# Kernel tuning notes

Hardware: AMD Instinct MI355X
Metric: run time of the kernel (lower is better)

## Reference

```python
import jax, jax.numpy as jnp
import numpy as np

NUM_WORDS = 100000
D_IN = 256

def setup_inputs() -> dict:
    key = jax.random.key(0)
    k1, k2 = jax.random.split(key)
    x = jax.random.normal(k1, (NUM_WORDS, D_IN), dtype=jnp.float32)
    # neighbor indices in [-1, NUM_WORDS); -1 means 'no neighbor' (masked out)
    indices = jax.random.randint(k2, (NUM_WORDS, 4), -1, NUM_WORDS, dtype=jnp.int64)
    return {"x": x, "indices": indices}

def reference(x, indices):
    # x: [N, D], indices: [N, 4] int (-1 -> masked neighbor)
    mask = (indices != -1)                               # [N, 4]
    safe_idx = jnp.maximum(indices, 0)                   # clamp -1 -> 0 like np.maximum in source
    gathered = x[safe_idx]                               # [N, 4, D]
    gathered = gathered * mask[..., None].astype(x.dtype)
    n, d = x.shape
    return jnp.concatenate([x, gathered.reshape(n, 4 * d)], axis=1)  # [N, 5*D]
```

## Files before the change

### kernel.cpp

```cpp
#include <hip/hip_runtime.h>


typedef float f32x4 __attribute__((ext_vector_type(4)));

#define D 256
#define D4 (D / 4)
#define OUTW (5 * D)
#define OUTW4 (OUTW / 4)
#define ROWS_PER_BLOCK 4

__global__ __launch_bounds__(256) void collect_kernel(
    const f32x4* __restrict__ x4,
    const int*   __restrict__ indices,
    f32x4*       __restrict__ out4,
    int n)
{
    const int wave = threadIdx.x >> 6;
    const int lane = threadIdx.x & 63;
    const int row  = blockIdx.x * ROWS_PER_BLOCK + wave;
    if (row >= n) return;

    const f32x4* xrow = x4 + (long)row * D4;
    f32x4* orow = out4 + (long)row * OUTW4;

    const int i0 = indices[row * 4 + 0];
    const int i1 = indices[row * 4 + 1];
    const int i2 = indices[row * 4 + 2];
    const int i3 = indices[row * 4 + 3];

    const f32x4 zero = (f32x4){0.f, 0.f, 0.f, 0.f};

    f32x4 v_self = __builtin_nontemporal_load(&xrow[lane]);
    f32x4 v0 = (i0 >= 0) ? x4[(long)i0 * D4 + lane] : zero;
    f32x4 v1 = (i1 >= 0) ? x4[(long)i1 * D4 + lane] : zero;
    f32x4 v2 = (i2 >= 0) ? x4[(long)i2 * D4 + lane] : zero;
    f32x4 v3 = (i3 >= 0) ? x4[(long)i3 * D4 + lane] : zero;

    __builtin_nontemporal_store(v_self, &orow[lane]);
    __builtin_nontemporal_store(v0, &orow[D4 * 1 + lane]);
    __builtin_nontemporal_store(v1, &orow[D4 * 2 + lane]);
    __builtin_nontemporal_store(v2, &orow[D4 * 3 + lane]);
    __builtin_nontemporal_store(v3, &orow[D4 * 4 + lane]);
}

extern "C" void kernel_launch(void* const* d_in, const int* in_sizes, int n_in,
                              void* d_out, int out_size, void* d_ws, size_t ws_size,
                              hipStream_t stream)
{
    const f32x4* x4 = (const f32x4*)d_in[0];
    const int* indices = (const int*)d_in[1];
    f32x4* out4 = (f32x4*)d_out;

    const int n = in_sizes[0] / D;

    dim3 block(256);
    dim3 grid((n + ROWS_PER_BLOCK - 1) / ROWS_PER_BLOCK);
    collect_kernel<<<grid, block, 0, stream>>>(x4, indices, out4, n);
}
```

Before: 150.8 us.

## Split gather into two passes over source-row halves for cache locality

Splits the gather into two kernel launches. Each launch only gathers neighbor rows whose index falls in one half of x, so the working set of gathered rows (about 51 MB per half) has a better chance of staying in the last-level cache. The first pass also copies the self rows and writes zeros for masked neighbors. The cost is a second launch, reading the indices twice, and more divergent branches per wave.

```diff
diff --git a/kernel.cpp b/kernel.cpp
--- a/kernel.cpp
+++ b/kernel.cpp
@@ -5,42 +5,56 @@
 
 #define D 256
 #define D4 (D / 4)
-#define OUTW (5 * D)
-#define OUTW4 (OUTW / 4)
+#define OUTW4 (5 * D / 4)
 #define ROWS_PER_BLOCK 4
 
-__global__ __launch_bounds__(256) void collect_kernel(
+__global__ __launch_bounds__(256) void collect_pass_kernel(
     const f32x4* __restrict__ x4,
     const int*   __restrict__ indices,
     f32x4*       __restrict__ out4,
-    int n)
+    int n, int seg_lo, int seg_hi, int do_self)
 {
     const int wave = threadIdx.x >> 6;
     const int lane = threadIdx.x & 63;
     const int row  = blockIdx.x * ROWS_PER_BLOCK + wave;
     if (row >= n) return;
 
-    const f32x4* xrow = x4 + (long)row * D4;
     f32x4* orow = out4 + (long)row * OUTW4;
 
-    const int i0 = indices[row * 4 + 0];
-    const int i1 = indices[row * 4 + 1];
-    const int i2 = indices[row * 4 + 2];
-    const int i3 = indices[row * 4 + 3];
+    int idx[4];
+    idx[0] = indices[row * 4 + 0];
+    idx[1] = indices[row * 4 + 1];
+    idx[2] = indices[row * 4 + 2];
+    idx[3] = indices[row * 4 + 3];
 
     const f32x4 zero = (f32x4){0.f, 0.f, 0.f, 0.f};
 
-    f32x4 v_self = __builtin_nontemporal_load(&xrow[lane]);
-    f32x4 v0 = (i0 >= 0) ? x4[(long)i0 * D4 + lane] : zero;
-    f32x4 v1 = (i1 >= 0) ? x4[(long)i1 * D4 + lane] : zero;
-    f32x4 v2 = (i2 >= 0) ? x4[(long)i2 * D4 + lane] : zero;
-    f32x4 v3 = (i3 >= 0) ? x4[(long)i3 * D4 + lane] : zero;
+    if (do_self) {
+        const f32x4* xrow = x4 + (long)row * D4;
+        f32x4 v_self;
+        if (row >= seg_lo && row < seg_hi) {
+            v_self = xrow[lane];
+        } else {
+            v_self = __builtin_nontemporal_load(&xrow[lane]);
+        }
+        __builtin_nontemporal_store(v_self, &orow[lane]);
 
-    __builtin_nontemporal_store(v_self, &orow[lane]);
-    __builtin_nontemporal_store(v0, &orow[D4 * 1 + lane]);
-    __builtin_nontemporal_store(v1, &orow[D4 * 2 + lane]);
-    __builtin_nontemporal_store(v2, &orow[D4 * 3 + lane]);
-    __builtin_nontemporal_store(v3, &orow[D4 * 4 + lane]);
+        #pragma unroll
+        for (int s = 0; s < 4; ++s) {
+            if (idx[s] < 0) {
+                __builtin_nontemporal_store(zero, &orow[D4 * (1 + s) + lane]);
+            }
+        }
+    }
+
+    #pragma unroll
+    for (int s = 0; s < 4; ++s) {
+        const int t = idx[s];
+        if (t >= seg_lo && t < seg_hi) {
+            f32x4 v = x4[(long)t * D4 + lane];
+            __builtin_nontemporal_store(v, &orow[D4 * (1 + s) + lane]);
+        }
+    }
 }
 
 extern "C" void kernel_launch(void* const* d_in, const int* in_sizes, int n_in,
@@ -52,8 +66,13 @@
     f32x4* out4 = (f32x4*)d_out;
 
     const int n = in_sizes[0] / D;
+    const int half = n / 2;
 
     dim3 block(256);
     dim3 grid((n + ROWS_PER_BLOCK - 1) / ROWS_PER_BLOCK);
-    collect_kernel<<<grid, block, 0, stream>>>(x4, indices, out4, n);
+
+    collect_pass_kernel<<<grid, block, 0, stream>>>(x4, indices, out4, n,
+                                                    0, half, 1);
+    collect_pass_kernel<<<grid, block, 0, stream>>>(x4, indices, out4, n,
+                                                    half, n, 0);
 }
```

Result: no change. 150.5 us (-0.2%).
